# Kernel tuning notes

Hardware: AMD Instinct MI355X
Metric: run time of the kernel (lower is better)

The kernel has to match this reference:

```python
import jax, jax.numpy as jnp
import numpy as np

H, W = 512, 512
N_GAUSS = 4096
T_EPS = 1e-3          # early-termination threshold from the torch loop
COV_DIAG = 25.0       # hardcoded cov_2d = eye(2) * 25 in rasterize_gaussians


def quat_to_rot(q):
    # standard (w, x, y, z) quaternion -> rotation matrix, with normalization
    q = q / jnp.linalg.norm(q)
    w, x, y, z = q[0], q[1], q[2], q[3]
    return jnp.array([
        [1 - 2 * (y * y + z * z), 2 * (x * y - w * z),     2 * (x * z + w * y)],
        [2 * (x * y + w * z),     1 - 2 * (x * x + z * z), 2 * (y * z - w * x)],
        [2 * (x * z - w * y),     2 * (y * z + w * x),     1 - 2 * (x * x + y * y)],
    ])


def setup_inputs() -> dict:
    key = jax.random.key(0)
    k0, k1, k2, k3 = jax.random.split(key, 4)
    xy = jax.random.uniform(k0, (N_GAUSS, 2), minval=-2.0, maxval=2.0)
    z = jax.random.uniform(k1, (N_GAUSS, 1), minval=4.0, maxval=10.0)
    positions = jnp.concatenate([xy, z], axis=-1)                    # [N,3], z>0
    colors = jax.random.uniform(k2, (N_GAUSS, 3))                    # [N,3] in [0,1]
    opacities = jax.random.uniform(k3, (N_GAUSS,)) * 0.5             # [N]
    quaternion = jnp.array([1.0, 0.05, 0.02, 0.01], dtype=jnp.float32)
    cam_position = jnp.zeros(3, dtype=jnp.float32)
    intrinsics = jnp.array([[500.0, 0.0, 256.0],
                            [0.0, 500.0, 256.0],
                            [0.0, 0.0, 1.0]], dtype=jnp.float32)
    background_color = jnp.zeros(3, dtype=jnp.float32)
    return {"positions": positions, "colors": colors, "opacities": opacities,
            "quaternion": quaternion, "cam_position": cam_position,
            "intrinsics": intrinsics, "background_color": background_color}


def _render(positions, colors, opacities, quaternion, cam_position, intrinsics,
            background_color):
    R = quat_to_rot(quaternion)                                      # [3,3]
    pos_cam = (positions - cam_position[None, :]) @ R.T              # [N,3]
    proj = pos_cam @ intrinsics.T                                    # [N,3]
    screen = proj[:, :2] / proj[:, 2:3]                              # [N,2]
    depths = proj[:, 2]                                              # [N]

    order = jnp.argsort(-depths)                                     # back-to-front
    centers_s = screen[order]
    colors_s = colors[order]
    opac_s = opacities[order]
    depth_s = pos_cam[order, 2]

    yy, xx = jnp.meshgrid(jnp.arange(H, dtype=jnp.float32),
                          jnp.arange(W, dtype=jnp.float32), indexing="ij")
    pix = jnp.stack([xx, yy], axis=-1)                               # [H,W,2] (x,y)

    init_color = jnp.broadcast_to(background_color[:, None, None], (3, H, W))
    carry0 = (init_color, jnp.zeros((H, W)), jnp.zeros((H, W)), jnp.ones((H, W)))

    def step(carry, g):
        color_acc, depth_acc, alpha_acc, T = carry
        center, color, opacity, depth = g
        # emulate the `if transmittance.max() < 1e-3: break` exactly: once T
        # saturates it is monotone, so masking all later contributions == break
        active = (jnp.max(T) >= T_EPS).astype(T.dtype)
        diff = pix - center[None, None, :]                           # [H,W,2]
        mahal = jnp.sum(diff * diff, axis=-1) / COV_DIAG             # cov_inv = I/25
        alpha = jnp.clip(jnp.exp(-0.5 * mahal) * opacity, 0.0, 1.0) * active
        ta = T * alpha
        color_acc = color_acc + ta[None, :, :] * color[:, None, None]
        depth_acc = depth_acc + ta * depth
        alpha_acc = alpha_acc + ta
        T = T * (1.0 - alpha)
        return (color_acc, depth_acc, alpha_acc, T), None

    (image, depth_map, alpha_map, _), _ = jax.lax.scan(
        step, carry0, (centers_s, colors_s, opac_s, depth_s))
    return image, depth_map, alpha_map


def reference(positions, colors, opacities, quaternion, cam_position, intrinsics,
              background_color):
    return _render(positions, colors, opacities, quaternion, cam_position,
                   intrinsics, background_color)
```

## Files before the change

kernel.cpp:

```cpp
#include <hip/hip_runtime.h>
#include <hip/hip_bf16.h>

#define N_GAUSS 4096
#define H 512
#define W 512
#define HW (H * W)
#define SEG 4
#define CULL2 1444.0f
#define MAXS 1024

__global__ __launch_bounds__(1024, 8) void render_all_kernel(
        const float* __restrict__ pos, const float* __restrict__ colors,
        const float* __restrict__ opac, const float* __restrict__ quat,
        const float* __restrict__ cam, const float* __restrict__ Km,
        const float* __restrict__ bg, float* __restrict__ out) {
    __shared__ __align__(16) float skey[MAXS + 4];
    __shared__ __align__(16) unsigned short sidxs[MAXS + 4];
    __shared__ __align__(16) float2 scxy[MAXS];
    __shared__ __align__(16) float4 scmp[MAXS];
    __shared__ __align__(16) float4 scol[MAXS];
    __shared__ float comb[SEG][6][256];
    __shared__ int scnt;

    int tid = threadIdx.x;
    int lane = tid & 63;
    int wave = tid >> 6;
    int seg = wave >> 2;
    int p = tid & 255;
    int tile = (blockIdx.x * 341) & 1023;
    int tx0 = (tile & 31) * 16, ty0 = (tile >> 5) * 16;
    float px = (float)(tx0 + (p & 15)), py = (float)(ty0 + (p >> 4));
    float tcx = tx0 + 7.5f, tcy = ty0 + 7.5f;

    if (tid == 0) scnt = 0;

    float qw = quat[0], qx = quat[1], qy = quat[2], qz = quat[3];
    float qn = 1.0f / sqrtf(qw * qw + qx * qx + qy * qy + qz * qz);
    qw *= qn; qx *= qn; qy *= qn; qz *= qn;
    float r00 = 1.f - 2.f * (qy * qy + qz * qz), r01 = 2.f * (qx * qy - qw * qz), r02 = 2.f * (qx * qz + qw * qy);
    float r10 = 2.f * (qx * qy + qw * qz), r11 = 1.f - 2.f * (qx * qx + qz * qz), r12 = 2.f * (qy * qz - qw * qx);
    float r20 = 2.f * (qx * qz - qw * qy), r21 = 2.f * (qy * qz + qw * qx), r22 = 1.f - 2.f * (qx * qx + qy * qy);
    float c0 = cam[0], c1 = cam[1], c2 = cam[2];
    float k0 = Km[0], k1 = Km[1], k2 = Km[2];
    float k3 = Km[3], k4 = Km[4], k5 = Km[5];
    float k6 = Km[6], k7 = Km[7], k8 = Km[8];

    __syncthreads();

    const float4* p4 = reinterpret_cast<const float4*>(pos);
    float4 pva = p4[3 * tid], pvb = p4[3 * tid + 1], pvc = p4[3 * tid + 2];
    float gxa[4] = {pva.x, pva.w, pvb.z, pvc.y};
    float gya[4] = {pva.y, pvb.x, pvb.w, pvc.z};
    float gza[4] = {pva.z, pvb.y, pvc.x, pvc.w};

    #pragma unroll
    for (int k = 0; k < 4; ++k) {
        int g = tid * 4 + k;
        float ax = gxa[k] - c0, ay = gya[k] - c1, az = gza[k] - c2;
        float X = r00 * ax + r01 * ay + r02 * az;
        float Y = r10 * ax + r11 * ay + r12 * az;
        float Z = r20 * ax + r21 * ay + r22 * az;
        float u = k0 * X + k1 * Y + k2 * Z;
        float v = k3 * X + k4 * Y + k5 * Z;
        float w = k6 * X + k7 * Y + k8 * Z;
        float sx = u / w, sy = v / w;
        float ddx = sx - tcx, ddy = sy - tcy;
        bool pred = (ddx * ddx + ddy * ddy <= CULL2);
        unsigned long long m = __ballot(pred ? 1 : 0);
        int base = 0;
        if (lane == 0) base = atomicAdd(&scnt, __popcll(m));
        base = __shfl(base, 0);
        if (pred) {
            int slot = base + __popcll(m & ((1ull << lane) - 1ull));
            if (slot < MAXS) {
                skey[slot] = Z;
                sidxs[slot] = (unsigned short)g;
                scxy[slot] = make_float2(sx, sy);
            }
        }
    }
    __syncthreads();
    int n = min(scnt, MAXS);
    if (tid < 4) { skey[n + tid] = -1e30f; sidxs[n + tid] = 0; }
    __syncthreads();

    if (tid < n) {
        float Zi = skey[tid];
        int idxi = sidxs[tid];
        int pad4 = (n + 3) & ~3;
        int r = 0;
        for (int j = 0; j < pad4; j += 4) {
            float4 kz = *reinterpret_cast<const float4*>(&skey[j]);
            ushort4 si = *reinterpret_cast<const ushort4*>(&sidxs[j]);
            r += (kz.x > Zi) || (kz.x == Zi && (int)si.x < idxi);
            r += (kz.y > Zi) || (kz.y == Zi && (int)si.y < idxi);
            r += (kz.z > Zi) || (kz.z == Zi && (int)si.z < idxi);
            r += (kz.w > Zi) || (kz.w == Zi && (int)si.w < idxi);
        }
        float2 xy = scxy[tid];
        scmp[r] = make_float4(xy.x, xy.y, Zi, opac[idxi]);
        scol[r] = make_float4(colors[3 * idxi], colors[3 * idxi + 1],
                              colors[3 * idxi + 2], 0.f);
    }
    __syncthreads();

    int q = (n + 3) >> 2;
    int beg = min(seg * q, n), end = min(beg + q, n);
    float T = 1.f, cr = 0.f, cg = 0.f, cb = 0.f, da = 0.f, aa = 0.f;
    #pragma unroll 2
    for (int g = beg; g < end; ++g) {
        float4 GA = scmp[g];
        float dx = px - GA.x, dy = py - GA.y;
        float al = __expf(-0.02f * (dx * dx + dy * dy)) * GA.w;
        float ta = T * al;
        float4 GC = scol[g];
        cr += ta * GC.x; cg += ta * GC.y; cb += ta * GC.z;
        da += ta * GA.z; aa += ta;
        T -= ta;
    }

    comb[seg][0][p] = cr;  comb[seg][1][p] = cg;  comb[seg][2][p] = cb;
    comb[seg][3][p] = da;  comb[seg][4][p] = aa;  comb[seg][5][p] = T;
    __syncthreads();
    if (seg == 0) {
        float r = 0.f, g2 = 0.f, b = 0.f, d = 0.f, a = 0.f;
        #pragma unroll
        for (int s = SEG - 1; s >= 0; --s) {
            float Ts = comb[s][5][p];
            r  = comb[s][0][p] + Ts * r;
            g2 = comb[s][1][p] + Ts * g2;
            b  = comb[s][2][p] + Ts * b;
            d  = comb[s][3][p] + Ts * d;
            a  = comb[s][4][p] + Ts * a;
        }
        int pid = (ty0 + (p >> 4)) * W + tx0 + (p & 15);
        out[pid]          = bg[0] + r;
        out[HW + pid]     = bg[1] + g2;
        out[2 * HW + pid] = bg[2] + b;
        out[3 * HW + pid] = d;
        out[4 * HW + pid] = a;
    }
}

extern "C" void kernel_launch(void* const* d_in, const int* in_sizes, int n_in,
                              void* d_out, int out_size, void* d_ws, size_t ws_size,
                              hipStream_t stream) {
    const float* positions = (const float*)d_in[0];
    const float* colors    = (const float*)d_in[1];
    const float* opacities = (const float*)d_in[2];
    const float* quat      = (const float*)d_in[3];
    const float* cam       = (const float*)d_in[4];
    const float* intr      = (const float*)d_in[5];
    const float* bg        = (const float*)d_in[6];
    float* out = (float*)d_out;
    (void)d_ws; (void)ws_size;

    render_all_kernel<<<dim3(1024), dim3(1024), 0, stream>>>(
        positions, colors, opacities, quat, cam, intr, bg, out);
}
```

Before: 106.5 us.

## Hoist gaussian projection into a prep kernel shared by all tiles

Adds a small pre-pass kernel that projects all 4096 gaussians once and packs screen xy, depth, opacity and colour into float4 workspace arrays. Before this, each of the 1024 render blocks redid the projection for every gaussian. The render kernel now reads the packed records, culls them, and scatters whole records into shared memory, which needs an extra barrier before the sorted write. This costs a second kernel launch and workspace traffic, and the render kernel must now wait for the prep kernel to finish.

```diff
diff --git a/kernel.cpp b/kernel.cpp
--- a/kernel.cpp
+++ b/kernel.cpp
@@ -9,15 +9,36 @@
 #define CULL2 1444.0f
 #define MAXS 1024
 
-__global__ __launch_bounds__(1024, 8) void render_all_kernel(
+
+__global__ __launch_bounds__(256) void prep_kernel(
         const float* __restrict__ pos, const float* __restrict__ colors,
         const float* __restrict__ opac, const float* __restrict__ quat,
         const float* __restrict__ cam, const float* __restrict__ Km,
+        float4* __restrict__ pxyz, float4* __restrict__ pcol) {
+    int i = blockIdx.x * 256 + threadIdx.x;
+    float qw = quat[0], qx = quat[1], qy = quat[2], qz = quat[3];
+    float qn = 1.0f / sqrtf(qw * qw + qx * qx + qy * qy + qz * qz);
+    qw *= qn; qx *= qn; qy *= qn; qz *= qn;
+    float r00 = 1.f - 2.f * (qy * qy + qz * qz), r01 = 2.f * (qx * qy - qw * qz), r02 = 2.f * (qx * qz + qw * qy);
+    float r10 = 2.f * (qx * qy + qw * qz), r11 = 1.f - 2.f * (qx * qx + qz * qz), r12 = 2.f * (qy * qz - qw * qx);
+    float r20 = 2.f * (qx * qz - qw * qy), r21 = 2.f * (qy * qz + qw * qx), r22 = 1.f - 2.f * (qx * qx + qy * qy);
+    float ax = pos[3 * i] - cam[0], ay = pos[3 * i + 1] - cam[1], az = pos[3 * i + 2] - cam[2];
+    float X = r00 * ax + r01 * ay + r02 * az;
+    float Y = r10 * ax + r11 * ay + r12 * az;
+    float Z = r20 * ax + r21 * ay + r22 * az;
+    float u = Km[0] * X + Km[1] * Y + Km[2] * Z;
+    float v = Km[3] * X + Km[4] * Y + Km[5] * Z;
+    float w = Km[6] * X + Km[7] * Y + Km[8] * Z;
+    pxyz[i] = make_float4(u / w, v / w, Z, opac[i]);
+    pcol[i] = make_float4(colors[3 * i], colors[3 * i + 1], colors[3 * i + 2], 0.f);
+}
+
+__global__ __launch_bounds__(1024, 8) void render_all_kernel(
+        const float4* __restrict__ pxyz, const float4* __restrict__ pcol,
         const float* __restrict__ bg, float* __restrict__ out) {
     __shared__ __align__(16) float skey[MAXS + 4];
     __shared__ __align__(16) unsigned short sidxs[MAXS + 4];
-    __shared__ __align__(16) float2 scxy[MAXS];
-    __shared__ __align__(16) float4 scmp[MAXS];
+    __shared__ __align__(16) float4 srec[MAXS];
     __shared__ __align__(16) float4 scol[MAXS];
     __shared__ float comb[SEG][6][256];
     __shared__ int scnt;
@@ -33,38 +54,13 @@
     float tcx = tx0 + 7.5f, tcy = ty0 + 7.5f;
 
     if (tid == 0) scnt = 0;
-
-    float qw = quat[0], qx = quat[1], qy = quat[2], qz = quat[3];
-    float qn = 1.0f / sqrtf(qw * qw + qx * qx + qy * qy + qz * qz);
-    qw *= qn; qx *= qn; qy *= qn; qz *= qn;
-    float r00 = 1.f - 2.f * (qy * qy + qz * qz), r01 = 2.f * (qx * qy - qw * qz), r02 = 2.f * (qx * qz + qw * qy);
-    float r10 = 2.f * (qx * qy + qw * qz), r11 = 1.f - 2.f * (qx * qx + qz * qz), r12 = 2.f * (qy * qz - qw * qx);
-    float r20 = 2.f * (qx * qz - qw * qy), r21 = 2.f * (qy * qz + qw * qx), r22 = 1.f - 2.f * (qx * qx + qy * qy);
-    float c0 = cam[0], c1 = cam[1], c2 = cam[2];
-    float k0 = Km[0], k1 = Km[1], k2 = Km[2];
-    float k3 = Km[3], k4 = Km[4], k5 = Km[5];
-    float k6 = Km[6], k7 = Km[7], k8 = Km[8];
-
     __syncthreads();
-
-    const float4* p4 = reinterpret_cast<const float4*>(pos);
-    float4 pva = p4[3 * tid], pvb = p4[3 * tid + 1], pvc = p4[3 * tid + 2];
-    float gxa[4] = {pva.x, pva.w, pvb.z, pvc.y};
-    float gya[4] = {pva.y, pvb.x, pvb.w, pvc.z};
-    float gza[4] = {pva.z, pvb.y, pvc.x, pvc.w};
 
     #pragma unroll
     for (int k = 0; k < 4; ++k) {
-        int g = tid * 4 + k;
-        float ax = gxa[k] - c0, ay = gya[k] - c1, az = gza[k] - c2;
-        float X = r00 * ax + r01 * ay + r02 * az;
-        float Y = r10 * ax + r11 * ay + r12 * az;
-        float Z = r20 * ax + r21 * ay + r22 * az;
-        float u = k0 * X + k1 * Y + k2 * Z;
-        float v = k3 * X + k4 * Y + k5 * Z;
-        float w = k6 * X + k7 * Y + k8 * Z;
-        float sx = u / w, sy = v / w;
-        float ddx = sx - tcx, ddy = sy - tcy;
+        int g = k * 1024 + tid;
+        float4 P = pxyz[g];
+        float ddx = P.x - tcx, ddy = P.y - tcy;
         bool pred = (ddx * ddx + ddy * ddy <= CULL2);
         unsigned long long m = __ballot(pred ? 1 : 0);
         int base = 0;
@@ -73,9 +69,9 @@
         if (pred) {
             int slot = base + __popcll(m & ((1ull << lane) - 1ull));
             if (slot < MAXS) {
-                skey[slot] = Z;
+                skey[slot] = P.z;
                 sidxs[slot] = (unsigned short)g;
-                scxy[slot] = make_float2(sx, sy);
+                srec[slot] = P;
             }
         }
     }
@@ -84,11 +80,13 @@
     if (tid < 4) { skey[n + tid] = -1e30f; sidxs[n + tid] = 0; }
     __syncthreads();
 
+    float4 rec;
+    int r = 0;
     if (tid < n) {
         float Zi = skey[tid];
         int idxi = sidxs[tid];
+        rec = srec[tid];
         int pad4 = (n + 3) & ~3;
-        int r = 0;
         for (int j = 0; j < pad4; j += 4) {
             float4 kz = *reinterpret_cast<const float4*>(&skey[j]);
             ushort4 si = *reinterpret_cast<const ushort4*>(&sidxs[j]);
@@ -97,10 +95,11 @@
             r += (kz.z > Zi) || (kz.z == Zi && (int)si.z < idxi);
             r += (kz.w > Zi) || (kz.w == Zi && (int)si.w < idxi);
         }
-        float2 xy = scxy[tid];
-        scmp[r] = make_float4(xy.x, xy.y, Zi, opac[idxi]);
-        scol[r] = make_float4(colors[3 * idxi], colors[3 * idxi + 1],
-                              colors[3 * idxi + 2], 0.f);
+    }
+    __syncthreads();
+    if (tid < n) {
+        srec[r] = rec;
+        scol[r] = pcol[sidxs[tid]];
     }
     __syncthreads();
 
@@ -109,7 +108,7 @@
     float T = 1.f, cr = 0.f, cg = 0.f, cb = 0.f, da = 0.f, aa = 0.f;
     #pragma unroll 2
     for (int g = beg; g < end; ++g) {
-        float4 GA = scmp[g];
+        float4 GA = srec[g];
         float dx = px - GA.x, dy = py - GA.y;
         float al = __expf(-0.02f * (dx * dx + dy * dy)) * GA.w;
         float ta = T * al;
@@ -123,22 +122,22 @@
     comb[seg][3][p] = da;  comb[seg][4][p] = aa;  comb[seg][5][p] = T;
     __syncthreads();
     if (seg == 0) {
-        float r = 0.f, g2 = 0.f, b = 0.f, d = 0.f, a = 0.f;
+        float r2 = 0.f, g2 = 0.f, b2 = 0.f, d2 = 0.f, a2 = 0.f;
         #pragma unroll
         for (int s = SEG - 1; s >= 0; --s) {
             float Ts = comb[s][5][p];
-            r  = comb[s][0][p] + Ts * r;
+            r2 = comb[s][0][p] + Ts * r2;
             g2 = comb[s][1][p] + Ts * g2;
-            b  = comb[s][2][p] + Ts * b;
-            d  = comb[s][3][p] + Ts * d;
-            a  = comb[s][4][p] + Ts * a;
+            b2 = comb[s][2][p] + Ts * b2;
+            d2 = comb[s][3][p] + Ts * d2;
+            a2 = comb[s][4][p] + Ts * a2;
         }
         int pid = (ty0 + (p >> 4)) * W + tx0 + (p & 15);
-        out[pid]          = bg[0] + r;
+        out[pid]          = bg[0] + r2;
         out[HW + pid]     = bg[1] + g2;
-        out[2 * HW + pid] = bg[2] + b;
-        out[3 * HW + pid] = d;
-        out[4 * HW + pid] = a;
+        out[2 * HW + pid] = bg[2] + b2;
+        out[3 * HW + pid] = d2;
+        out[4 * HW + pid] = a2;
     }
 }
 
@@ -153,8 +152,12 @@
     const float* intr      = (const float*)d_in[5];
     const float* bg        = (const float*)d_in[6];
     float* out = (float*)d_out;
-    (void)d_ws; (void)ws_size;
 
+    float4* pxyz = (float4*)d_ws;
+    float4* pcol = (float4*)((char*)d_ws + 65536);
+
+    prep_kernel<<<dim3(16), dim3(256), 0, stream>>>(
+        positions, colors, opacities, quat, cam, intr, pxyz, pcol);
     render_all_kernel<<<dim3(1024), dim3(1024), 0, stream>>>(
-        positions, colors, opacities, quat, cam, intr, bg, out);
+        pxyz, pcol, bg, out);
 }
```

Result: no change. 105.1 us (-1.3%).
